# Kernel tuning notes

Measured on AMD Instinct MI355X. Metric: run time of the kernel, lower is better.

## Reference

```python
import jax, jax.numpy as jnp
import numpy as np


def setup_inputs() -> dict:
    key = jax.random.key(0)
    ks = jax.random.split(key, 8)
    B, T, N = 8, 8192, 256
    x = jax.random.normal(ks[0], (B, T, N), dtype=jnp.float32)
    # stable-ish LRU params: nu_log/theta_log as in the torch init
    u1 = jax.random.uniform(ks[1], (N,), dtype=jnp.float32)
    r_min, r_max = 0.4, 0.9
    nu_log = jnp.log(-0.5 * jnp.log(u1 * (r_max + r_min) * (r_max - r_min) + r_min ** 2))
    u2 = jax.random.uniform(ks[2], (N,), dtype=jnp.float32)
    theta_log = jnp.log(2.0 * np.pi * u2)
    L_mod = jnp.exp(-jnp.exp(nu_log))
    gamma_log = jnp.log(jnp.sqrt(1.0 - jnp.square(L_mod)))
    s2 = 1.0 / np.sqrt(2 * N)
    s1 = 1.0 / np.sqrt(N)
    B_re = jax.random.normal(ks[3], (N, N), dtype=jnp.float32) * s2
    B_im = jax.random.normal(ks[4], (N, N), dtype=jnp.float32) * s2
    C_re = jax.random.normal(ks[5], (N, N), dtype=jnp.float32) * s1
    C_im = jax.random.normal(ks[6], (N, N), dtype=jnp.float32) * s1
    return {"x": x, "nu_log": nu_log, "theta_log": theta_log, "gamma_log": gamma_log,
            "B_re": B_re, "B_im": B_im, "C_re": C_re, "C_im": C_im}


def _binop(e_i, e_j):
    # associative combine for diagonal linear recurrence h_j = a_j * h_i + b_j
    a_i, b_i = e_i
    a_j, b_j = e_j
    return a_j * a_i, a_j * b_i + b_j


def reference(x, nu_log, theta_log, gamma_log, B_re, B_im, C_re, C_im):
    # Lambda (diagonal complex state transition)
    L_mod = jnp.exp(-jnp.exp(nu_log))                     # [N]
    theta = jnp.exp(theta_log)                            # [N]
    L_diag = (L_mod * jnp.cos(theta) + 1j * (L_mod * jnp.sin(theta)))  # complex64 [N]
    # normalized input projection
    B_norm = (B_re + 1j * B_im) * jnp.exp(gamma_log)[:, None]          # [N, N]
    Bu = jnp.einsum('btn,mn->btm', x.astype(B_norm.dtype), B_norm)     # [B, T, N] complex
    L_elems = jnp.broadcast_to(L_diag, Bu.shape)                        # [B, T, N]
    # parallel associative scan over time axis (zero initial state)
    _, states = jax.lax.associative_scan(_binop, (L_elems, Bu), axis=1)
    C = C_re + 1j * C_im
    return jnp.einsum('btn,mn->btm', states, C).real
```

## Files before the change

### kernel.cpp

```cpp
#include <hip/hip_runtime.h>

#define NB 8
#define TT 8192
#define NN 256
#define CH 64
#define BT (NB*TT)
#define NCHUNK (BT/CH)
#define GPB (TT/CH)

typedef float f4 __attribute__((ext_vector_type(4)));
typedef unsigned u4 __attribute__((ext_vector_type(4)));
typedef short b8 __attribute__((ext_vector_type(8)));

static __device__ __forceinline__ ushort f2bf(float f) {
  union { float f; unsigned u; } v; v.f = f;
  return (ushort)((v.u + 0x7fffu + ((v.u >> 16) & 1u)) >> 16);
}
static __device__ __forceinline__ float bf2f(ushort h) {
  union { unsigned u; float f; } v; v.u = ((unsigned)h) << 16; return v.f;
}

__global__ void k_setup(const float* __restrict__ nu_log, const float* __restrict__ theta_log,
                        const float* __restrict__ gamma_log,
                        const float* __restrict__ B_re, const float* __restrict__ B_im,
                        const float* __restrict__ C_re, const float* __restrict__ C_im,
                        float2* __restrict__ Lc, float2* __restrict__ LCH,
                        float2* __restrict__ Lpow,
                        ushort* __restrict__ BnRe, ushort* __restrict__ BnIm,
                        ushort* __restrict__ CRe, ushort* __restrict__ CIm) {
  int bid = blockIdx.x, tid = threadIdx.x;
  if (bid < NN) {
    int m = bid, n = tid;
    float g = expf(gamma_log[m]);
    int idx = m * NN + n;
    BnRe[idx] = f2bf(B_re[idx] * g);
    BnIm[idx] = f2bf(B_im[idx] * g);
    CRe[idx]  = f2bf(C_re[idx]);
    CIm[idx]  = f2bf(-C_im[idx]);
  } else {
    int m = tid;
    float Lmod = expf(-expf(nu_log[m]));
    float th = expf(theta_log[m]);
    float lre = Lmod * cosf(th), lim = Lmod * sinf(th);
    Lc[m] = make_float2(lre, lim);
    float pr = 1.f, pi = 0.f;
    for (int k = 0; k < CH; ++k) {
      Lpow[(size_t)(CH - 1 - k) * NN + m] = make_float2(pr, pi);
      float npr = pr * lre - pi * lim;
      pi = pr * lim + pi * lre;
      pr = npr;
    }
    LCH[m] = make_float2(pr, pi);
  }
}

static __device__ __forceinline__ void stage_x_f32(const float* __restrict__ xt,
                                                   char* lds, int tid) {
#pragma unroll
  for (int i = 0; i < 16; ++i) {
    int fi = i * 1024 + tid * 4;
    f4 w = *(const f4*)(xt + fi);
    int r = fi >> 8, c = fi & 255;
    int dst = r * 1024 + ((c * 4) ^ ((r & 7) << 4));
    *(f4*)(lds + dst) = w;
  }
}

static __device__ __forceinline__ void gemm1_ldsx(const char* lds,
                                                  const ushort* __restrict__ BnRe,
                                                  const ushort* __restrict__ BnIm,
                                                  int tid, f4 accRe[4][4], f4 accIm[4][4]) {
  int lane = tid & 63, wid = tid >> 6;
  int lr = lane & 15, lg = lane >> 4;
  int mq = wid * 64;
  for (int ks = 0; ks < 8; ++ks) {
    int k0 = ks * 32 + lg * 8;
    b8 a[4];
    for (int mf = 0; mf < 4; ++mf) {
      int r = mf * 16 + lr;
      int sw = (r & 7) << 4;
      const char* base = lds + r * 1024;
      f4 x0 = *(const f4*)(base + ((k0 * 4) ^ sw));
      f4 x1 = *(const f4*)(base + ((k0 * 4 + 16) ^ sw));
      b8 t;
      t[0] = (short)f2bf(x0[0]); t[1] = (short)f2bf(x0[1]);
      t[2] = (short)f2bf(x0[2]); t[3] = (short)f2bf(x0[3]);
      t[4] = (short)f2bf(x1[0]); t[5] = (short)f2bf(x1[1]);
      t[6] = (short)f2bf(x1[2]); t[7] = (short)f2bf(x1[3]);
      a[mf] = t;
    }
    for (int nf = 0; nf < 4; ++nf) {
      int mrow = mq + nf * 16 + lr;
      b8 br = *(const b8*)(BnRe + (size_t)mrow * NN + k0);
      b8 bi = *(const b8*)(BnIm + (size_t)mrow * NN + k0);
      for (int mf = 0; mf < 4; ++mf) {
        accRe[mf][nf] = __builtin_amdgcn_mfma_f32_16x16x32_bf16(a[mf], br, accRe[mf][nf], 0, 0, 0);
        accIm[mf][nf] = __builtin_amdgcn_mfma_f32_16x16x32_bf16(a[mf], bi, accIm[mf][nf], 0, 0, 0);
      }
    }
  }
}

__global__ __launch_bounds__(256) void k_carry(const float* __restrict__ x,
                                               const ushort* __restrict__ BnRe,
                                               const ushort* __restrict__ BnIm,
                                               const float2* __restrict__ Lc,
                                               const float2* __restrict__ Lpow,
                                               float2* __restrict__ carry) {
  __shared__ char lds[65536];
  int cid = blockIdx.x, tid = threadIdx.x;
  int lane = tid & 63, wid = tid >> 6;
  int lr = lane & 15, lg = lane >> 4;
  int mq = wid * 64;

  float2 pL1[4], pL4[4], pL8[4], pL16[4];
  for (int nf = 0; nf < 4; ++nf) {
    int c = mq + nf * 16 + lr;
    pL1[nf]  = Lc[c];
    pL4[nf]  = Lpow[(size_t)(CH - 1 - 4)  * NN + c];
    pL8[nf]  = Lpow[(size_t)(CH - 1 - 8)  * NN + c];
    pL16[nf] = Lpow[(size_t)(CH - 1 - 16) * NN + c];
  }

  stage_x_f32(x + (size_t)cid * CH * NN, lds, tid);
  __syncthreads();

  f4 accRe[4][4], accIm[4][4];
  for (int i = 0; i < 4; ++i)
    for (int j = 0; j < 4; ++j) { accRe[i][j] = (f4)0.f; accIm[i][j] = (f4)0.f; }
  gemm1_ldsx(lds, BnRe, BnIm, tid, accRe, accIm);

  for (int nf = 0; nf < 4; ++nf) {
    float2 L1 = pL1[nf], L4 = pL4[nf], L8 = pL8[nf], L16 = pL16[nf];
    float Cr[4], Ci[4];
    for (int mf = 0; mf < 4; ++mf) {
      float cr = accRe[mf][nf][0], ci = accIm[mf][nf][0];
      for (int q = 1; q < 4; ++q) {
        float nr = L1.x * cr - L1.y * ci + accRe[mf][nf][q];
        ci = L1.x * ci + L1.y * cr + accIm[mf][nf][q];
        cr = nr;
      }
      Cr[mf] = cr; Ci[mf] = ci;
    }
    float Hx = 0.f, Hy = 0.f;
    for (int mf = 0; mf < 4; ++mf) {
      float tx = __shfl_up(Cr[mf], 16, 64), ty = __shfl_up(Ci[mf], 16, 64);
      float m1 = (lg >= 1) ? 1.f : 0.f;
      float ax = Cr[mf] + m1 * (L4.x * tx - L4.y * ty);
      float ay = Ci[mf] + m1 * (L4.x * ty + L4.y * tx);
      float ux = __shfl_up(ax, 32, 64), uy = __shfl_up(ay, 32, 64);
      float m2 = (lg >= 2) ? 1.f : 0.f;
      float Ix = ax + m2 * (L8.x * ux - L8.y * uy);
      float Iy = ay + m2 * (L8.x * uy + L8.y * ux);
      float Qx = __shfl(Ix, lr + 48, 64), Qy = __shfl(Iy, lr + 48, 64);
      float nHx = Qx + L16.x * Hx - L16.y * Hy;
      Hy = Qy + L16.x * Hy + L16.y * Hx;
      Hx = nHx;
    }
    if (lg == 0) carry[(size_t)cid * NN + mq + nf * 16 + lr] = make_float2(Hx, Hy);
  }
}

__global__ void k_seed(float2* __restrict__ carrySeed, const float2* __restrict__ LCH) {
  int b = blockIdx.x, m = threadIdx.x;
  float2 LC = LCH[m];
  float hr = 0.f, hi = 0.f;
  size_t base = (size_t)b * GPB * NN + m;
  float2 c = carrySeed[base];
  for (int g = 0; g < GPB; ++g) {
    size_t idx = base + (size_t)g * NN;
    float2 cn = (g + 1 < GPB) ? carrySeed[idx + NN] : make_float2(0.f, 0.f);
    carrySeed[idx] = make_float2(hr, hi);
    float nr = LC.x * hr - LC.y * hi + c.x;
    hi = LC.x * hi + LC.y * hr + c.y;
    hr = nr;
    c = cn;
  }
}

__global__ __launch_bounds__(256) void k_out(const float* __restrict__ x,
                                             const ushort* __restrict__ BnRe,
                                             const ushort* __restrict__ BnIm,
                                             const float2* __restrict__ Lc,
                                             const float2* __restrict__ seed,
                                             const ushort* __restrict__ CRe,
                                             const ushort* __restrict__ CIm,
                                             const float2* __restrict__ Lpow,
                                             float* __restrict__ out) {
  __shared__ char lds[65536];
  int cid = blockIdx.x, tid = threadIdx.x;
  size_t rowbase = (size_t)cid * CH;
  int lane = tid & 63, wid = tid >> 6;
  int lr = lane & 15, lg = lane >> 4;
  int mq = wid * 64;

  float2 pL1[4], pL4[4], pL8[4], pL16[4], pw4[4], psd[4];
  for (int nf = 0; nf < 4; ++nf) {
    int c = mq + nf * 16 + lr;
    pL1[nf]  = Lc[c];
    pL4[nf]  = Lpow[(size_t)(CH - 1 - 4)  * NN + c];
    pL8[nf]  = Lpow[(size_t)(CH - 1 - 8)  * NN + c];
    pL16[nf] = Lpow[(size_t)(CH - 1 - 16) * NN + c];
    pw4[nf]  = (lg == 0) ? make_float2(1.f, 0.f)
                         : Lpow[(size_t)(CH - 1 - 4 * lg) * NN + c];
    psd[nf]  = seed[(size_t)cid * NN + c];
  }

  stage_x_f32(x + rowbase * NN, lds, tid);
  __syncthreads();

  f4 accRe[4][4], accIm[4][4];
  for (int i = 0; i < 4; ++i)
    for (int j = 0; j < 4; ++j) { accRe[i][j] = (f4)0.f; accIm[i][j] = (f4)0.f; }
  gemm1_ldsx(lds, BnRe, BnIm, tid, accRe, accIm);

  for (int nf = 0; nf < 4; ++nf) {
    float2 L1 = pL1[nf], L4 = pL4[nf], L8 = pL8[nf], L16 = pL16[nf];
    float2 w4 = pw4[nf], sd = psd[nf];

    float Cr[4], Ci[4];
    for (int mf = 0; mf < 4; ++mf) {
      for (int q = 1; q < 4; ++q) {
        float sr_ = L1.x * accRe[mf][nf][q-1] - L1.y * accIm[mf][nf][q-1] + accRe[mf][nf][q];
        float si_ = L1.x * accIm[mf][nf][q-1] + L1.y * accRe[mf][nf][q-1] + accIm[mf][nf][q];
        accRe[mf][nf][q] = sr_; accIm[mf][nf][q] = si_;
      }
      Cr[mf] = accRe[mf][nf][3]; Ci[mf] = accIm[mf][nf][3];
    }

    float Er[4], Ei[4], Qr[4], Qi[4];
    for (int mf = 0; mf < 4; ++mf) {
      float tx = __shfl_up(Cr[mf], 16, 64), ty = __shfl_up(Ci[mf], 16, 64);
      float m1 = (lg >= 1) ? 1.f : 0.f;
      float ax = Cr[mf] + m1 * (L4.x * tx - L4.y * ty);
      float ay = Ci[mf] + m1 * (L4.x * ty + L4.y * tx);
      float ux = __shfl_up(ax, 32, 64), uy = __shfl_up(ay, 32, 64);
      float m2 = (lg >= 2) ? 1.f : 0.f;
      float Ix = ax + m2 * (L8.x * ux - L8.y * uy);
      float Iy = ay + m2 * (L8.x * uy + L8.y * ux);
      float ex = __shfl_up(Ix, 16, 64), ey = __shfl_up(Iy, 16, 64);
      Er[mf] = m1 * ex; Ei[mf] = m1 * ey;
      Qr[mf] = __shfl(Ix, lr + 48, 64); Qi[mf] = __shfl(Iy, lr + 48, 64);
    }

    float Hx = sd.x, Hy = sd.y;
    for (int mf = 0; mf < 4; ++mf) {
      float Zx = Er[mf] + w4.x * Hx - w4.y * Hy;
      float Zy = Ei[mf] + w4.x * Hy + w4.y * Hx;
      float Wx = L1.x, Wy = L1.y;
      for (int q = 0; q < 4; ++q) {
        float hr_ = accRe[mf][nf][q] + Wx * Zx - Wy * Zy;
        float hi_ = accIm[mf][nf][q] + Wx * Zy + Wy * Zx;
        accRe[mf][nf][q] = hr_; accIm[mf][nf][q] = hi_;
        if (q < 3) { float nWx = Wx * L1.x - Wy * L1.y; Wy = Wx * L1.y + Wy * L1.x; Wx = nWx; }
      }
      float nHx = Qr[mf] + L16.x * Hx - L16.y * Hy;
      Hy = Qi[mf] + L16.x * Hy + L16.y * Hx;
      Hx = nHx;
    }
  }
  __syncthreads();

  for (int mf = 0; mf < 4; ++mf)
    for (int nf = 0; nf < 4; ++nf)
      for (int r = 0; r < 4; ++r) {
        int row = mf * 16 + lg * 4 + r;
        int col = mq + nf * 16 + lr;
        unsigned p = (unsigned)f2bf(accRe[mf][nf][r]) | ((unsigned)f2bf(accIm[mf][nf][r]) << 16);
        int off = row * 1024 + ((col * 4) ^ ((row & 7) << 4));
        *(unsigned*)(lds + off) = p;
      }
  __syncthreads();

  f4 acc[4][4];
  for (int i = 0; i < 4; ++i)
    for (int j = 0; j < 4; ++j) acc[i][j] = (f4)0.f;

  for (int ks = 0; ks < 8; ++ks) {
    int k0 = ks * 32 + lg * 8;
    b8 ar[4], ai[4];
    for (int mf = 0; mf < 4; ++mf) {
      int row = mf * 16 + lr;
      int m4 = (row & 7) << 4;
      const char* base = lds + row * 1024;
      u4 p0 = *(const u4*)(base + ((k0 * 4) ^ m4));
      u4 p1 = *(const u4*)(base + ((k0 * 4 + 16) ^ m4));
      b8 tr, ti;
      tr[0] = (short)(p0[0] & 0xffffu); ti[0] = (short)(p0[0] >> 16);
      tr[1] = (short)(p0[1] & 0xffffu); ti[1] = (short)(p0[1] >> 16);
      tr[2] = (short)(p0[2] & 0xffffu); ti[2] = (short)(p0[2] >> 16);
      tr[3] = (short)(p0[3] & 0xffffu); ti[3] = (short)(p0[3] >> 16);
      tr[4] = (short)(p1[0] & 0xffffu); ti[4] = (short)(p1[0] >> 16);
      tr[5] = (short)(p1[1] & 0xffffu); ti[5] = (short)(p1[1] >> 16);
      tr[6] = (short)(p1[2] & 0xffffu); ti[6] = (short)(p1[2] >> 16);
      tr[7] = (short)(p1[3] & 0xffffu); ti[7] = (short)(p1[3] >> 16);
      ar[mf] = tr; ai[mf] = ti;
    }
    for (int nf = 0; nf < 4; ++nf) {
      int m = mq + nf * 16 + lr;
      b8 cr = *(const b8*)(CRe + (size_t)m * NN + k0);
      b8 ci = *(const b8*)(CIm + (size_t)m * NN + k0);
      for (int mf = 0; mf < 4; ++mf) {
        acc[mf][nf] = __builtin_amdgcn_mfma_f32_16x16x32_bf16(ar[mf], cr, acc[mf][nf], 0, 0, 0);
        acc[mf][nf] = __builtin_amdgcn_mfma_f32_16x16x32_bf16(ai[mf], ci, acc[mf][nf], 0, 0, 0);
      }
    }
  }
  for (int mf = 0; mf < 4; ++mf)
    for (int nf = 0; nf < 4; ++nf)
      for (int r = 0; r < 4; ++r) {
        size_t t = rowbase + mf * 16 + lg * 4 + r;
        out[t * NN + mq + nf * 16 + lr] = acc[mf][nf][r];
      }
}

extern "C" void kernel_launch(void* const* d_in, const int* in_sizes, int n_in,
                              void* d_out, int out_size, void* d_ws, size_t ws_size,
                              hipStream_t stream) {
  const float* x         = (const float*)d_in[0];
  const float* nu_log    = (const float*)d_in[1];
  const float* theta_log = (const float*)d_in[2];
  const float* gamma_log = (const float*)d_in[3];
  const float* B_re      = (const float*)d_in[4];
  const float* B_im      = (const float*)d_in[5];
  const float* C_re      = (const float*)d_in[6];
  const float* C_im      = (const float*)d_in[7];
  float* out = (float*)d_out;

  char* ws = (char*)d_ws;
  float2*  carrySeed = (float2*)(ws + 0);
  float2*  Lc   = (float2*)(ws + 2097152);
  float2*  LCH  = (float2*)(ws + 2099200);
  ushort*  BnRe = (ushort*)(ws + 2101248);
  ushort*  BnIm = (ushort*)(ws + 2232320);
  ushort*  CRe  = (ushort*)(ws + 2363392);
  ushort*  CIm  = (ushort*)(ws + 2494464);
  float2*  Lpow = (float2*)(ws + 2625536);

  hipLaunchKernelGGL(k_setup, dim3(NN + 1), dim3(NN), 0, stream,
                     nu_log, theta_log, gamma_log, B_re, B_im, C_re, C_im,
                     Lc, LCH, Lpow, BnRe, BnIm, CRe, CIm);
  hipLaunchKernelGGL(k_carry, dim3(NCHUNK), dim3(256), 0, stream,
                     x, BnRe, BnIm, Lc, Lpow, carrySeed);
  hipLaunchKernelGGL(k_seed, dim3(NB), dim3(NN), 0, stream, carrySeed, LCH);
  hipLaunchKernelGGL(k_out, dim3(NCHUNK), dim3(256), 0, stream,
                     x, BnRe, BnIm, Lc, carrySeed, CRe, CIm, Lpow, out);
}
```

Measured before the change: 178.5 us.

## Stage x as bf16 in LDS and batch carry-seed loads

The x tile is converted from fp32 to bf16 once while it is staged into LDS. This halves LDS usage from 64KB to 32KB and removes the repeated per-fragment conversion that each wave did in the GEMM loop. The GEMM now reads 8 bf16 values directly from LDS as the MFMA operand. Separately, the sequential seed scan now prefetches 16 carries at a time, so its dependent global-load latency is hidden. Smaller LDS may raise occupancy. k_out likely still uses 64KB of LDS for other stages, which caps the gain there.

Measured after the change: 181.5 us. No clear change (+1.7%).

```diff
diff --git a/kernel.cpp b/kernel.cpp
--- a/kernel.cpp
+++ b/kernel.cpp
@@ -10,6 +10,7 @@
 
 typedef float f4 __attribute__((ext_vector_type(4)));
 typedef unsigned u4 __attribute__((ext_vector_type(4)));
+typedef short b4 __attribute__((ext_vector_type(4)));
 typedef short b8 __attribute__((ext_vector_type(8)));
 
 static __device__ __forceinline__ ushort f2bf(float f) {
@@ -54,15 +55,18 @@
   }
 }
 
-static __device__ __forceinline__ void stage_x_f32(const float* __restrict__ xt,
-                                                   char* lds, int tid) {
+static __device__ __forceinline__ void stage_x_bf16(const float* __restrict__ xt,
+                                                    char* lds, int tid) {
 #pragma unroll
   for (int i = 0; i < 16; ++i) {
     int fi = i * 1024 + tid * 4;
     f4 w = *(const f4*)(xt + fi);
     int r = fi >> 8, c = fi & 255;
-    int dst = r * 1024 + ((c * 4) ^ ((r & 7) << 4));
-    *(f4*)(lds + dst) = w;
+    int dst = r * 512 + ((c * 2) ^ ((r & 7) << 4));
+    b4 p;
+    p[0] = (short)f2bf(w[0]); p[1] = (short)f2bf(w[1]);
+    p[2] = (short)f2bf(w[2]); p[3] = (short)f2bf(w[3]);
+    *(b4*)(lds + dst) = p;
   }
 }
 
@@ -78,16 +82,7 @@
     b8 a[4];
     for (int mf = 0; mf < 4; ++mf) {
       int r = mf * 16 + lr;
-      int sw = (r & 7) << 4;
-      const char* base = lds + r * 1024;
-      f4 x0 = *(const f4*)(base + ((k0 * 4) ^ sw));
-      f4 x1 = *(const f4*)(base + ((k0 * 4 + 16) ^ sw));
-      b8 t;
-      t[0] = (short)f2bf(x0[0]); t[1] = (short)f2bf(x0[1]);
-      t[2] = (short)f2bf(x0[2]); t[3] = (short)f2bf(x0[3]);
-      t[4] = (short)f2bf(x1[0]); t[5] = (short)f2bf(x1[1]);
-      t[6] = (short)f2bf(x1[2]); t[7] = (short)f2bf(x1[3]);
-      a[mf] = t;
+      a[mf] = *(const b8*)(lds + r * 512 + ((k0 * 2) ^ ((r & 7) << 4)));
     }
     for (int nf = 0; nf < 4; ++nf) {
       int mrow = mq + nf * 16 + lr;
@@ -107,7 +102,7 @@
                                                const float2* __restrict__ Lc,
                                                const float2* __restrict__ Lpow,
                                                float2* __restrict__ carry) {
-  __shared__ char lds[65536];
+  __shared__ char lds[32768];
   int cid = blockIdx.x, tid = threadIdx.x;
   int lane = tid & 63, wid = tid >> 6;
   int lr = lane & 15, lg = lane >> 4;
@@ -122,7 +117,7 @@
     pL16[nf] = Lpow[(size_t)(CH - 1 - 16) * NN + c];
   }
 
-  stage_x_f32(x + (size_t)cid * CH * NN, lds, tid);
+  stage_x_bf16(x + (size_t)cid * CH * NN, lds, tid);
   __syncthreads();
 
   f4 accRe[4][4], accIm[4][4];
@@ -166,15 +161,19 @@
   float2 LC = LCH[m];
   float hr = 0.f, hi = 0.f;
   size_t base = (size_t)b * GPB * NN + m;
-  float2 c = carrySeed[base];
-  for (int g = 0; g < GPB; ++g) {
-    size_t idx = base + (size_t)g * NN;
-    float2 cn = (g + 1 < GPB) ? carrySeed[idx + NN] : make_float2(0.f, 0.f);
-    carrySeed[idx] = make_float2(hr, hi);
-    float nr = LC.x * hr - LC.y * hi + c.x;
-    hi = LC.x * hi + LC.y * hr + c.y;
-    hr = nr;
-    c = cn;
+  for (int g0 = 0; g0 < GPB; g0 += 16) {
+    float2 buf[16];
+#pragma unroll
+    for (int j = 0; j < 16; ++j)
+      buf[j] = carrySeed[base + (size_t)(g0 + j) * NN];
+#pragma unroll
+    for (int j = 0; j < 16; ++j) {
+      carrySeed[base + (size_t)(g0 + j) * NN] = make_float2(hr, hi);
+      float2 c = buf[j];
+      float nr = LC.x * hr - LC.y * hi + c.x;
+      hi = LC.x * hi + LC.y * hr + c.y;
+      hr = nr;
+    }
   }
 }
 
@@ -206,7 +205,7 @@
     psd[nf]  = seed[(size_t)cid * NN + c];
   }
 
-  stage_x_f32(x + rowbase * NN, lds, tid);
+  stage_x_bf16(x + rowbase * NN, lds, tid);
   __syncthreads();
 
   f4 accRe[4][4], accIm[4][4];
```
